# Optimization experiments

Hardware: AMD Instinct MI355X
Metric: run time of the kernel (lower is better)

Reference implementation:

```python
import jax, jax.numpy as jnp
import numpy as np

B, T, D, H, L = 8, 150, 30, 5, 3
HD = D // H  # 6
ORIG = (300, 74, 35)


def setup_inputs() -> dict:
    key = jax.random.key(0)
    ks = iter(jax.random.split(key, 40))
    def g(shape, s=0.05):
        return jax.random.normal(next(ks), shape, dtype=jnp.float32) * s
    return {
        "x_l": g((B, T, ORIG[0]), 1.0),
        "x_a": g((B, T, ORIG[1]), 1.0),
        "x_v": g((B, T, ORIG[2]), 1.0),
        "Wl": g((D, ORIG[0])),
        "Wa": g((D, ORIG[1])),
        "Wv": g((D, ORIG[2])),
        "in_w": g((2, L, 3 * D, D)),
        "in_b": jnp.zeros((2, L, 3 * D), jnp.float32),
        "out_w": g((2, L, D, D)),
        "out_b": jnp.zeros((2, L, D), jnp.float32),
        "lin1_w": g((2, L, 4 * D, D)),
        "lin1_b": jnp.zeros((2, L, 4 * D), jnp.float32),
        "lin2_w": g((2, L, D, 4 * D)),
        "lin2_b": jnp.zeros((2, L, D), jnp.float32),
        "n1_g": jnp.ones((2, L, D), jnp.float32),
        "n1_b": jnp.zeros((2, L, D), jnp.float32),
        "n2_g": jnp.ones((2, L, D), jnp.float32),
        "n2_b": jnp.zeros((2, L, D), jnp.float32),
        "p1_w": g((2 * D, 2 * D)),
        "p1_b": jnp.zeros((2 * D,), jnp.float32),
        "p2_w": g((2 * D, 2 * D)),
        "p2_b": jnp.zeros((2 * D,), jnp.float32),
        "ow": g((1, 2 * D)),
        "ob": jnp.zeros((1,), jnp.float32),
    }


def _ln(x, g, b, eps=1e-5):
    m = x.mean(-1, keepdims=True)
    v = jnp.var(x, axis=-1, keepdims=True)  # biased var, matches torch LayerNorm
    return (x - m) * jax.lax.rsqrt(v + eps) * g + b


def _heads(x):  # [Tt, B, D] -> [B*H, Tt, HD]
    Tt = x.shape[0]
    return x.reshape(Tt, B * H, HD).transpose(1, 0, 2)


def _layer(x, xk, xv, p):
    iw, ib, ow, ob, w1, b1, w2, b2, g1, bb1, g2, bb2 = p
    res = x
    xn, kn, vn = _ln(x, g1, bb1), _ln(xk, g1, bb1), _ln(xv, g1, bb1)
    q = (xn @ iw[:D].T + ib[:D]) * (HD ** -0.5)
    k = kn @ iw[D:2 * D].T + ib[D:2 * D]
    v = vn @ iw[2 * D:].T + ib[2 * D:]
    qh, kh, vh = _heads(q), _heads(k), _heads(v)
    # trilinear scores: [B*H, Tq, Tk, Tv]
    aw = jnp.einsum('iat,ibt,ict->iabc', qh, kh, vh)
    fused = aw.mean(-1) + aw.max(-1)          # fuse over value axis -> [B*H, Tq, Tk]
    fused = jax.nn.softmax(fused, axis=-1)
    attn = jnp.einsum('iab,ibt->iat', fused, qh)  # NB: original bmm uses q, not v
    attn = attn.transpose(1, 0, 2).reshape(-1, B, D)
    x = res + (attn @ ow.T + ob)
    res = x
    xn = _ln(x, g2, bb2)
    x = jax.nn.relu(xn @ w1.T + b1) @ w2.T + b2
    return res + x


def reference(x_l, x_a, x_v, Wl, Wa, Wv, in_w, in_b, out_w, out_b,
              lin1_w, lin1_b, lin2_w, lin2_b, n1_g, n1_b, n2_g, n2_b,
              p1_w, p1_b, p2_w, p2_b, ow, ob):
    pl = (x_l @ Wl.T).transpose(1, 0, 2)  # [T, B, D] (conv1d k=1, no bias)
    pa = (x_a @ Wa.T).transpose(1, 0, 2)
    pv = (x_v @ Wv.T).transpose(1, 0, 2)
    hs = []
    for s, (kk, vv) in enumerate(((pa, pv), (pv, pa))):
        h = pl
        for l in range(L):
            p = (in_w[s, l], in_b[s, l], out_w[s, l], out_b[s, l],
                 lin1_w[s, l], lin1_b[s, l], lin2_w[s, l], lin2_b[s, l],
                 n1_g[s, l], n1_b[s, l], n2_g[s, l], n2_b[s, l])
            h = _layer(h, kk, vv, p)
        hs.append(h[-1])  # last timestep [B, D]
    last_hs = jnp.concatenate(hs, axis=1)  # [B, 2D]
    proj = jax.nn.relu(last_hs @ p1_w.T + p1_b) @ p2_w.T + p2_b + last_hs
    out = proj @ ow.T + ob
    return (out, last_hs)
```

## Files before the change

kernel.cpp:

```cpp
#include <hip/hip_runtime.h>
#include <math.h>

#define BB 8
#define TT 150
#define DD 30
#define HH 5
#define HD 6
#define LL 3
#define NI 40
#define ROWF (TT*BB*DD)
#define RSTR 8
#define NR 152

typedef _Float16 half8 __attribute__((ext_vector_type(8)));
typedef float f32x16 __attribute__((ext_vector_type(16)));

__device__ __forceinline__ float wsum(float v) {
    #pragma unroll
    for (int m = 32; m > 0; m >>= 1) v += __shfl_xor(v, m, 64);
    return v;
}

__global__ __launch_bounds__(256) void proj3_kernel(
    const float* __restrict__ x_l, const float* __restrict__ x_a, const float* __restrict__ x_v,
    const float* __restrict__ Wl, const float* __restrict__ Wa, const float* __restrict__ Wv,
    float* __restrict__ pl, float* __restrict__ pa, float* __restrict__ pv) {
    int w = threadIdx.x >> 6, lane = threadIdx.x & 63;
    int unit = blockIdx.x * 4 + w;
    int which = unit / 1200, rowu = unit % 1200;
    int t = rowu / BB, b = rowu % BB;
    const float* x = which == 0 ? x_l : (which == 1 ? x_a : x_v);
    const float* W = which == 0 ? Wl : (which == 1 ? Wa : Wv);
    float* out = which == 0 ? pl : (which == 1 ? pa : pv);
    int Cin = which == 0 ? 300 : (which == 1 ? 74 : 35);
    __shared__ float xr[4][304];
    const float* xp = x + ((size_t)b * TT + t) * Cin;
    for (int j = lane; j < Cin; j += 64) xr[w][j] = xp[j];
    __syncthreads();
    int d = lane >> 1, jh = lane & 1;
    int h1 = Cin >> 1;
    int j0 = jh ? h1 : 0, j1 = jh ? Cin : h1;
    const float* wr = W + (size_t)(d < DD ? d : 0) * Cin;
    float acc = 0.f;
    for (int j = j0; j < j1; j++) acc += xr[w][j] * wr[j];
    acc += __shfl_xor(acc, 1, 64);
    if (jh == 0 && d < DD) out[t * (BB * DD) + b * DD + d] = acc;
}

__global__ __launch_bounds__(256) void lnqkv_kernel(
    const float* __restrict__ h, const float* __restrict__ pl,
    const float* __restrict__ pa, const float* __restrict__ pv,
    const float* __restrict__ in_w, const float* __restrict__ in_b,
    const float* __restrict__ n1g, const float* __restrict__ n1b, int l,
    float* __restrict__ q, float* __restrict__ k, float* __restrict__ v) {
    int w = threadIdx.x >> 6, lane = threadIdx.x & 63;
    int unit = blockIdx.x * 4 + w;
    int s = unit / 1200, tb = unit % 1200;
    int t = tb / BB, b = tb % BB;
    const float* xk = (s == 0) ? pa : pv;
    const float* xv = (s == 0) ? pv : pa;
    int po = s * LL + l;
    const float* iw = in_w + (size_t)po * 90 * 30;
    const float* ib = in_b + (size_t)po * 90;
    const float* g  = n1g + (size_t)po * 30;
    const float* bbv = n1b + (size_t)po * 30;
    __shared__ float xn[4][3][30];
    const float* rows[3];
    rows[0] = (l == 0) ? (pl + (size_t)tb * 30) : (h + (size_t)s * ROWF + (size_t)tb * 30);
    rows[1] = xk + (size_t)tb * 30;
    rows[2] = xv + (size_t)tb * 30;
    for (int r = 0; r < 3; r++) {
        float xval = (lane < 30) ? rows[r][lane] : 0.f;
        float mean = wsum(xval) * (1.f / 30.f);
        float dv = (lane < 30) ? (xval - mean) : 0.f;
        float var = wsum(dv * dv) * (1.f / 30.f);
        float inv = rsqrtf(var + 1e-5f);
        if (lane < 30) xn[w][r][lane] = dv * inv * g[lane] + bbv[lane];
    }
    __syncthreads();
    for (int o = lane; o < 90; o += 64) {
        int which = o / 30, dd = o % 30;
        const float* wr = iw + o * 30;
        const float* xr = xn[w][which];
        float acc = 0.f;
        #pragma unroll 6
        for (int j = 0; j < 30; j++) acc += wr[j] * xr[j];
        acc += ib[o];
        if (which == 0) acc *= 0.40824829046386307f;
        int i = b * HH + dd / HD, hd = dd % HD;
        float* dst = (which == 0) ? q : ((which == 1) ? k : v);
        dst[((size_t)s * NI + i) * (TT * HD) + t * HD + hd] = acc;
    }
}

__global__ __launch_bounds__(256) void scoreffn_kernel(
    const float* __restrict__ q, const float* __restrict__ k, const float* __restrict__ v,
    const float* __restrict__ pl,
    const float* __restrict__ out_w, const float* __restrict__ out_b,
    const float* __restrict__ l1w, const float* __restrict__ l1b,
    const float* __restrict__ l2w, const float* __restrict__ l2b,
    const float* __restrict__ n2g, const float* __restrict__ n2b, int l,
    float* __restrict__ h) {
    int blk = blockIdx.x;
    int s = blk / 304;
    int rem = blk % 304;
    int b = rem / 38;
    int g = rem % 38;
    int tid = threadIdx.x;
    int wv = tid >> 6, lane = tid & 63;
    int lo = lane & 31, hf = lane >> 5;

    __shared__ __align__(16) _Float16 qsh[HH][NR * RSTR];
    __shared__ __align__(16) _Float16 ksh[HH][NR * RSTR];
    __shared__ __align__(16) _Float16 vsh[HH][NR * RSTR];
    __shared__ float attnS[4][32];
    __shared__ float xnS[4][32];
    __shared__ float hidS[4][128];

    int* qz = (int*)&qsh[0][0];
    int* kz = (int*)&ksh[0][0];
    int* vz = (int*)&vsh[0][0];
    for (int idx = tid; idx < HH * NR * RSTR / 2; idx += 256) {
        qz[idx] = 0; kz[idx] = 0; vz[idx] = 0;
    }
    __syncthreads();
    const float* qg = q + (size_t)(s * NI + b * HH) * (TT * HD);
    const float* kg = k + (size_t)(s * NI + b * HH) * (TT * HD);
    const float* vg = v + (size_t)(s * NI + b * HH) * (TT * HD);
    for (int idx = tid; idx < HH * TT * HD; idx += 256) {
        int h5 = idx / (TT * HD);
        int rr = (idx % (TT * HD)) / HD;
        int t = idx % HD;
        int dst = rr * RSTR + t;
        qsh[h5][dst] = (_Float16)qg[idx];
        ksh[h5][dst] = (_Float16)kg[idx];
        vsh[h5][dst] = (_Float16)vg[idx];
    }
    __syncthreads();
    for (int h5 = wv; h5 < HH; h5 += 4) {
        float v6[6] = {0.f, 0.f, 0.f, 0.f, 0.f, 0.f};
        for (int c = lane; c < TT; c += 64) {
            #pragma unroll
            for (int t = 0; t < 6; t++) v6[t] += (float)vsh[h5][c * RSTR + t];
        }
        #pragma unroll
        for (int m = 32; m > 0; m >>= 1) {
            #pragma unroll
            for (int t = 0; t < 6; t++) v6[t] += __shfl_xor(v6[t], m, 64);
        }
        if (lane < 6) vsh[h5][TT * RSTR + lane] = (_Float16)(v6[lane] * (1.f / TT));
    }
    __syncthreads();

    int a = g * 4 + wv;
    bool alive = (a < TT);

    f32x16 zacc;
    #pragma unroll
    for (int j = 0; j < 16; j++) zacc[j] = 0.f;
    half8 zero8;
    #pragma unroll
    for (int t = 0; t < 8; t++) zero8[t] = (_Float16)0.f;

    if (alive) {
        for (int h5 = 0; h5 < HH; h5++) {
            const _Float16* kbase = qsh[0];
            (void)kbase;
            half8 qav = *(const half8*)&qsh[h5][a * RSTR];
            half8 bfrag[5], afrag[5];
            #pragma unroll
            for (int nt = 0; nt < 5; nt++) {
                int rr = nt * 32 + lo;
                int rc = rr < 151 ? rr : 151;
                half8 kf = *(const half8*)&ksh[h5][rc * RSTR];
                half8 vf = *(const half8*)&vsh[h5][rc * RSTR];
                bfrag[nt] = hf ? zero8 : kf;
                afrag[nt] = hf ? zero8 : (vf * qav);
            }
            float fsc[5];
            #pragma unroll
            for (int nb = 0; nb < 5; nb++) {
                float rm = -INFINITY;
                #pragma unroll
                for (int ma = 0; ma < 4; ma++) {
                    f32x16 acc = __builtin_amdgcn_mfma_f32_32x32x16_f16(afrag[ma], bfrag[nb], zacc, 0, 0, 0);
                    float m = fmaxf(acc[0], acc[1]);
                    #pragma unroll
                    for (int j = 2; j < 16; j += 2) m = fmaxf(fmaxf(m, acc[j]), acc[j + 1]);
                    rm = fmaxf(rm, m);
                }
                f32x16 a4 = __builtin_amdgcn_mfma_f32_32x32x16_f16(afrag[4], bfrag[nb], zacc, 0, 0, 0);
                float m4 = fmaxf(a4[0], a4[1]);
                #pragma unroll
                for (int j = 2; j < 10; j += 2) m4 = fmaxf(fmaxf(m4, a4[j]), a4[j + 1]);
                float ext = (hf == 0) ? fmaxf(a4[10], a4[11]) : -INFINITY;
                rm = fmaxf(rm, fmaxf(m4, ext));
                float om = __shfl_xor(a4[10], 32, 64);
                float mn = hf ? a4[10] : om;
                rm = fmaxf(rm, __shfl_xor(rm, 32, 64));
                int bcol = nb * 32 + lo;
                fsc[nb] = (bcol < TT) ? (mn + rm) : -INFINITY;
            }
            float m = fsc[0];
            #pragma unroll
            for (int nb = 1; nb < 5; nb++) m = fmaxf(m, fsc[nb]);
            #pragma unroll
            for (int msk = 16; msk > 0; msk >>= 1) m = fmaxf(m, __shfl_xor(m, msk, 64));
            float e[5], es = 0.f;
            #pragma unroll
            for (int nb = 0; nb < 5; nb++) { e[nb] = __expf(fsc[nb] - m); es += e[nb]; }
            #pragma unroll
            for (int msk = 16; msk > 0; msk >>= 1) es += __shfl_xor(es, msk, 64);
            float acc6[6] = {0.f, 0.f, 0.f, 0.f, 0.f, 0.f};
            #pragma unroll
            for (int nb = 0; nb < 5; nb++) {
                int bcol = nb * 32 + lo;
                int bi = (bcol < TT) ? bcol : 0;
                float wgt = e[nb];
                half8 qrow = *(const half8*)&qsh[h5][bi * RSTR];
                #pragma unroll
                for (int t = 0; t < 6; t++) acc6[t] += wgt * (float)qrow[t];
            }
            #pragma unroll
            for (int msk = 16; msk > 0; msk >>= 1) {
                #pragma unroll
                for (int t = 0; t < 6; t++) acc6[t] += __shfl_xor(acc6[t], msk, 64);
            }
            if (lane == 0) {
                float inv = 1.f / es;
                #pragma unroll
                for (int t = 0; t < 6; t++) attnS[wv][h5 * 6 + t] = acc6[t] * inv;
            }
        }

        int tb = a * BB + b;
        int po = s * LL + l;
        const float* ow = out_w + (size_t)po * 900;
        const float* ob = out_b + (size_t)po * 30;
        const float* w1 = l1w + (size_t)po * 120 * 30;
        const float* b1 = l1b + (size_t)po * 120;
        const float* w2 = l2w + (size_t)po * 30 * 120;
        const float* b2 = l2b + (size_t)po * 30;
        const float* gg = n2g + (size_t)po * 30;
        const float* bbv = n2b + (size_t)po * 30;
        float* hrow = h + (size_t)s * ROWF + (size_t)tb * 30;
        const float* res = (l == 0) ? (pl + (size_t)tb * 30) : hrow;
        float x1v = 0.f;
        if (lane < 30) {
            const float* wr = ow + lane * 30;
            float acc = 0.f;
            #pragma unroll 6
            for (int j = 0; j < 30; j++) acc += wr[j] * attnS[wv][j];
            x1v = res[lane] + acc + ob[lane];
        }
        float mean = wsum(x1v) * (1.f / 30.f);
        float dv = (lane < 30) ? (x1v - mean) : 0.f;
        float var = wsum(dv * dv) * (1.f / 30.f);
        float inv = rsqrtf(var + 1e-5f);
        if (lane < 30) xnS[wv][lane] = dv * inv * gg[lane] + bbv[lane];
        for (int o = lane; o < 120; o += 64) {
            const float* wr = w1 + o * 30;
            float acc = 0.f;
            #pragma unroll 6
            for (int j = 0; j < 30; j++) acc += wr[j] * xnS[wv][j];
            hidS[wv][o] = fmaxf(acc + b1[o], 0.f);
        }
        if (lane < 30) {
            const float* wr = w2 + lane * 120;
            float acc = 0.f;
            #pragma unroll 8
            for (int j = 0; j < 120; j++) acc += wr[j] * hidS[wv][j];
            hrow[lane] = x1v + acc + b2[lane];
        }
    }
}

__global__ __launch_bounds__(256) void head_kernel(
    const float* __restrict__ h,
    const float* __restrict__ p1w, const float* __restrict__ p1b,
    const float* __restrict__ p2w, const float* __restrict__ p2b,
    const float* __restrict__ ow, const float* __restrict__ ob,
    float* __restrict__ out) {
    int tid = threadIdx.x;
    __shared__ float lh[480], hid[480], pr[480];
    for (int idx = tid; idx < 480; idx += 256) {
        int b = idx / 60, j = idx % 60;
        int s = j / 30, d = j % 30;
        float vv = h[(size_t)s * ROWF + 149 * (BB * DD) + b * DD + d];
        lh[idx] = vv;
        out[8 + idx] = vv;
    }
    __syncthreads();
    for (int idx = tid; idx < 480; idx += 256) {
        int b = idx / 60, o = idx % 60;
        const float* wr = p1w + o * 60;
        float acc = p1b[o];
        for (int j = 0; j < 60; j++) acc += wr[j] * lh[b * 60 + j];
        hid[idx] = fmaxf(acc, 0.f);
    }
    __syncthreads();
    for (int idx = tid; idx < 480; idx += 256) {
        int b = idx / 60, d = idx % 60;
        const float* wr = p2w + d * 60;
        float acc = p2b[d];
        for (int j = 0; j < 60; j++) acc += wr[j] * hid[b * 60 + j];
        pr[idx] = acc + lh[idx];
    }
    __syncthreads();
    if (tid < 8) {
        float acc = ob[0];
        for (int j = 0; j < 60; j++) acc += pr[tid * 60 + j] * ow[j];
        out[tid] = acc;
    }
}

extern "C" void kernel_launch(void* const* d_in, const int* in_sizes, int n_in,
                              void* d_out, int out_size, void* d_ws, size_t ws_size,
                              hipStream_t stream) {
    const float* x_l   = (const float*)d_in[0];
    const float* x_a   = (const float*)d_in[1];
    const float* x_v   = (const float*)d_in[2];
    const float* Wl    = (const float*)d_in[3];
    const float* Wa    = (const float*)d_in[4];
    const float* Wv    = (const float*)d_in[5];
    const float* in_w  = (const float*)d_in[6];
    const float* in_b  = (const float*)d_in[7];
    const float* out_w = (const float*)d_in[8];
    const float* out_b = (const float*)d_in[9];
    const float* l1w   = (const float*)d_in[10];
    const float* l1b   = (const float*)d_in[11];
    const float* l2w   = (const float*)d_in[12];
    const float* l2b   = (const float*)d_in[13];
    const float* n1g   = (const float*)d_in[14];
    const float* n1b   = (const float*)d_in[15];
    const float* n2g   = (const float*)d_in[16];
    const float* n2b   = (const float*)d_in[17];
    const float* p1w   = (const float*)d_in[18];
    const float* p1b   = (const float*)d_in[19];
    const float* p2w   = (const float*)d_in[20];
    const float* p2b   = (const float*)d_in[21];
    const float* oww   = (const float*)d_in[22];
    const float* obb   = (const float*)d_in[23];

    float* ws = (float*)d_ws;
    float* pl = ws;
    float* pa = ws + 36000;
    float* pv = ws + 72000;
    float* h  = ws + 108000;
    float* q  = ws + 180000;
    float* kk = ws + 252000;
    float* vv = ws + 324000;

    proj3_kernel<<<900, 256, 0, stream>>>(x_l, x_a, x_v, Wl, Wa, Wv, pl, pa, pv);

    for (int l = 0; l < LL; l++) {
        lnqkv_kernel<<<600, 256, 0, stream>>>(h, pl, pa, pv, in_w, in_b, n1g, n1b, l, q, kk, vv);
        scoreffn_kernel<<<608, 256, 0, stream>>>(q, kk, vv, pl, out_w, out_b,
                                                 l1w, l1b, l2w, l2b, n2g, n2b, l, h);
    }
    head_kernel<<<1, 256, 0, stream>>>(h, p1w, p1b, p2w, p2b, oww, obb, (float*)d_out);
}
```

Before: 280.4 us.

## Split fused score+FFN kernel into per-head score and FFN kernels; stage weights in LDS

The fused score/FFN kernel is split in two. The score kernel now runs one block per (stream, head, group of 8 query rows), so it loads only one head's Q/K/V into LDS and keeps the K/V fragments in registers across two query rows per wave. A separate FFN kernel reads the attention output from a new workspace buffer. The projection, QKV and FFN kernels also stage their weight matrices in shared memory, padded to avoid bank conflicts. This gives more parallelism and less redundant staging, at the cost of an extra launch per layer and a global round trip for the attention output.

```diff
diff --git a/kernel.cpp b/kernel.cpp
--- a/kernel.cpp
+++ b/kernel.cpp
@@ -25,22 +25,27 @@
     const float* __restrict__ x_l, const float* __restrict__ x_a, const float* __restrict__ x_v,
     const float* __restrict__ Wl, const float* __restrict__ Wa, const float* __restrict__ Wv,
     float* __restrict__ pl, float* __restrict__ pa, float* __restrict__ pv) {
+    int blk = blockIdx.x;
+    int which = blk / 300;
     int w = threadIdx.x >> 6, lane = threadIdx.x & 63;
-    int unit = blockIdx.x * 4 + w;
-    int which = unit / 1200, rowu = unit % 1200;
+    int rowu = (blk % 300) * 4 + w;
     int t = rowu / BB, b = rowu % BB;
     const float* x = which == 0 ? x_l : (which == 1 ? x_a : x_v);
     const float* W = which == 0 ? Wl : (which == 1 ? Wa : Wv);
     float* out = which == 0 ? pl : (which == 1 ? pa : pv);
     int Cin = which == 0 ? 300 : (which == 1 ? 74 : 35);
+    int cst = Cin + ((Cin & 1) ? 0 : 1);
+    __shared__ float WS[30 * 301];
     __shared__ float xr[4][304];
+    for (int j = threadIdx.x; j < DD * Cin; j += 256)
+        WS[(j / Cin) * cst + (j % Cin)] = W[j];
     const float* xp = x + ((size_t)b * TT + t) * Cin;
     for (int j = lane; j < Cin; j += 64) xr[w][j] = xp[j];
     __syncthreads();
     int d = lane >> 1, jh = lane & 1;
     int h1 = Cin >> 1;
     int j0 = jh ? h1 : 0, j1 = jh ? Cin : h1;
-    const float* wr = W + (size_t)(d < DD ? d : 0) * Cin;
+    const float* wr = WS + (size_t)(d < DD ? d : 0) * cst;
     float acc = 0.f;
     for (int j = j0; j < j1; j++) acc += xr[w][j] * wr[j];
     acc += __shfl_xor(acc, 1, 64);
@@ -53,9 +58,10 @@
     const float* __restrict__ in_w, const float* __restrict__ in_b,
     const float* __restrict__ n1g, const float* __restrict__ n1b, int l,
     float* __restrict__ q, float* __restrict__ k, float* __restrict__ v) {
+    int blk = blockIdx.x;
+    int s = blk / 300;
     int w = threadIdx.x >> 6, lane = threadIdx.x & 63;
-    int unit = blockIdx.x * 4 + w;
-    int s = unit / 1200, tb = unit % 1200;
+    int tb = (blk % 300) * 4 + w;
     int t = tb / BB, b = tb % BB;
     const float* xk = (s == 0) ? pa : pv;
     const float* xv = (s == 0) ? pv : pa;
@@ -64,7 +70,9 @@
     const float* ib = in_b + (size_t)po * 90;
     const float* g  = n1g + (size_t)po * 30;
     const float* bbv = n1b + (size_t)po * 30;
+    __shared__ float iwS[2700];
     __shared__ float xn[4][3][30];
+    for (int j = threadIdx.x; j < 2700; j += 256) iwS[j] = iw[j];
     const float* rows[3];
     rows[0] = (l == 0) ? (pl + (size_t)tb * 30) : (h + (size_t)s * ROWF + (size_t)tb * 30);
     rows[1] = xk + (size_t)tb * 30;
@@ -80,7 +88,7 @@
     __syncthreads();
     for (int o = lane; o < 90; o += 64) {
         int which = o / 30, dd = o % 30;
-        const float* wr = iw + o * 30;
+        const float* wr = iwS + o * 30;
         const float* xr = xn[w][which];
         float acc = 0.f;
         #pragma unroll 6
@@ -93,185 +101,195 @@
     }
 }
 
-__global__ __launch_bounds__(256) void scoreffn_kernel(
+__global__ __launch_bounds__(256) void score_kernel(
     const float* __restrict__ q, const float* __restrict__ k, const float* __restrict__ v,
-    const float* __restrict__ pl,
+    float* __restrict__ attn) {
+    int blk = blockIdx.x;
+    int s = blk / 760;
+    int rem = blk % 760;
+    int i = rem / 19;
+    int g = rem % 19;
+    int tid = threadIdx.x;
+    int wv = tid >> 6, lane = tid & 63;
+    int lo = lane & 31, hf = lane >> 5;
+
+    __shared__ __align__(16) _Float16 qsh[NR * RSTR];
+    __shared__ __align__(16) _Float16 ksh[NR * RSTR];
+    __shared__ __align__(16) _Float16 vsh[NR * RSTR];
+
+    int* qz = (int*)qsh; int* kz = (int*)ksh; int* vz = (int*)vsh;
+    for (int idx = tid; idx < NR * RSTR / 2; idx += 256) {
+        qz[idx] = 0; kz[idx] = 0; vz[idx] = 0;
+    }
+    __syncthreads();
+    const float* qg = q + (size_t)(s * NI + i) * (TT * HD);
+    const float* kg = k + (size_t)(s * NI + i) * (TT * HD);
+    const float* vg = v + (size_t)(s * NI + i) * (TT * HD);
+    for (int idx = tid; idx < TT * HD; idx += 256) {
+        int dst = (idx / HD) * RSTR + (idx % HD);
+        qsh[dst] = (_Float16)qg[idx];
+        ksh[dst] = (_Float16)kg[idx];
+        vsh[dst] = (_Float16)vg[idx];
+    }
+    __syncthreads();
+    if (wv == 0) {
+        float v6[6] = {0.f, 0.f, 0.f, 0.f, 0.f, 0.f};
+        for (int c = lane; c < TT; c += 64) {
+            #pragma unroll
+            for (int t = 0; t < 6; t++) v6[t] += (float)vsh[c * RSTR + t];
+        }
+        #pragma unroll
+        for (int m = 32; m > 0; m >>= 1) {
+            #pragma unroll
+            for (int t = 0; t < 6; t++) v6[t] += __shfl_xor(v6[t], m, 64);
+        }
+        if (lane < 6) vsh[TT * RSTR + lane] = (_Float16)(v6[lane] * (1.f / TT));
+    }
+    __syncthreads();
+
+    f32x16 zacc;
+    #pragma unroll
+    for (int j = 0; j < 16; j++) zacc[j] = 0.f;
+    half8 zero8;
+    #pragma unroll
+    for (int t = 0; t < 8; t++) zero8[t] = (_Float16)0.f;
+
+    half8 bfrag[5], vhalf[5];
+    #pragma unroll
+    for (int nt = 0; nt < 5; nt++) {
+        int rr = nt * 32 + lo;
+        int rc = rr < 151 ? rr : 151;
+        half8 kf = *(const half8*)&ksh[rc * RSTR];
+        half8 vf = *(const half8*)&vsh[rc * RSTR];
+        bfrag[nt] = hf ? zero8 : kf;
+        vhalf[nt] = hf ? zero8 : vf;
+    }
+
+    for (int ap = 0; ap < 2; ap++) {
+        int a = g * 8 + wv * 2 + ap;
+        if (a >= TT) break;
+        half8 qav = *(const half8*)&qsh[a * RSTR];
+        half8 afrag[5];
+        #pragma unroll
+        for (int nt = 0; nt < 5; nt++) afrag[nt] = vhalf[nt] * qav;
+
+        float fsc[5];
+        #pragma unroll
+        for (int nb = 0; nb < 5; nb++) {
+            float rm = -INFINITY;
+            #pragma unroll
+            for (int ma = 0; ma < 4; ma++) {
+                f32x16 acc = __builtin_amdgcn_mfma_f32_32x32x16_f16(afrag[ma], bfrag[nb], zacc, 0, 0, 0);
+                float m = fmaxf(acc[0], acc[1]);
+                #pragma unroll
+                for (int j = 2; j < 16; j += 2) m = fmaxf(fmaxf(m, acc[j]), acc[j + 1]);
+                rm = fmaxf(rm, m);
+            }
+            f32x16 a4 = __builtin_amdgcn_mfma_f32_32x32x16_f16(afrag[4], bfrag[nb], zacc, 0, 0, 0);
+            float m4 = fmaxf(a4[0], a4[1]);
+            #pragma unroll
+            for (int j = 2; j < 10; j += 2) m4 = fmaxf(fmaxf(m4, a4[j]), a4[j + 1]);
+            float ext = (hf == 0) ? fmaxf(a4[10], a4[11]) : -INFINITY;
+            rm = fmaxf(rm, fmaxf(m4, ext));
+            float om = __shfl_xor(a4[10], 32, 64);
+            float mn = hf ? a4[10] : om;
+            rm = fmaxf(rm, __shfl_xor(rm, 32, 64));
+            int bcol = nb * 32 + lo;
+            fsc[nb] = (bcol < TT) ? (mn + rm) : -INFINITY;
+        }
+        float m = fsc[0];
+        #pragma unroll
+        for (int nb = 1; nb < 5; nb++) m = fmaxf(m, fsc[nb]);
+        #pragma unroll
+        for (int msk = 16; msk > 0; msk >>= 1) m = fmaxf(m, __shfl_xor(m, msk, 64));
+        float e[5], es = 0.f;
+        #pragma unroll
+        for (int nb = 0; nb < 5; nb++) { e[nb] = __expf(fsc[nb] - m); es += e[nb]; }
+        #pragma unroll
+        for (int msk = 16; msk > 0; msk >>= 1) es += __shfl_xor(es, msk, 64);
+        float acc6[6] = {0.f, 0.f, 0.f, 0.f, 0.f, 0.f};
+        #pragma unroll
+        for (int nb = 0; nb < 5; nb++) {
+            int bcol = nb * 32 + lo;
+            int bi = (bcol < TT) ? bcol : 0;
+            float wgt = e[nb];
+            half8 qrow = *(const half8*)&qsh[bi * RSTR];
+            #pragma unroll
+            for (int t = 0; t < 6; t++) acc6[t] += wgt * (float)qrow[t];
+        }
+        #pragma unroll
+        for (int msk = 16; msk > 0; msk >>= 1) {
+            #pragma unroll
+            for (int t = 0; t < 6; t++) acc6[t] += __shfl_xor(acc6[t], msk, 64);
+        }
+        if (lane == 0) {
+            float inv = 1.f / es;
+            int bo = i / HH, ho = i % HH;
+            float* dst = attn + (size_t)s * ROWF + a * (BB * DD) + bo * DD + ho * HD;
+            #pragma unroll
+            for (int t = 0; t < 6; t++) dst[t] = acc6[t] * inv;
+        }
+    }
+}
+
+__global__ __launch_bounds__(256) void ffn_kernel(
+    const float* __restrict__ attn, const float* __restrict__ pl,
     const float* __restrict__ out_w, const float* __restrict__ out_b,
     const float* __restrict__ l1w, const float* __restrict__ l1b,
     const float* __restrict__ l2w, const float* __restrict__ l2b,
     const float* __restrict__ n2g, const float* __restrict__ n2b, int l,
     float* __restrict__ h) {
     int blk = blockIdx.x;
-    int s = blk / 304;
-    int rem = blk % 304;
-    int b = rem / 38;
-    int g = rem % 38;
-    int tid = threadIdx.x;
-    int wv = tid >> 6, lane = tid & 63;
-    int lo = lane & 31, hf = lane >> 5;
-
-    __shared__ __align__(16) _Float16 qsh[HH][NR * RSTR];
-    __shared__ __align__(16) _Float16 ksh[HH][NR * RSTR];
-    __shared__ __align__(16) _Float16 vsh[HH][NR * RSTR];
-    __shared__ float attnS[4][32];
-    __shared__ float xnS[4][32];
-    __shared__ float hidS[4][128];
-
-    int* qz = (int*)&qsh[0][0];
-    int* kz = (int*)&ksh[0][0];
-    int* vz = (int*)&vsh[0][0];
-    for (int idx = tid; idx < HH * NR * RSTR / 2; idx += 256) {
-        qz[idx] = 0; kz[idx] = 0; vz[idx] = 0;
-    }
-    __syncthreads();
-    const float* qg = q + (size_t)(s * NI + b * HH) * (TT * HD);
-    const float* kg = k + (size_t)(s * NI + b * HH) * (TT * HD);
-    const float* vg = v + (size_t)(s * NI + b * HH) * (TT * HD);
-    for (int idx = tid; idx < HH * TT * HD; idx += 256) {
-        int h5 = idx / (TT * HD);
-        int rr = (idx % (TT * HD)) / HD;
-        int t = idx % HD;
-        int dst = rr * RSTR + t;
-        qsh[h5][dst] = (_Float16)qg[idx];
-        ksh[h5][dst] = (_Float16)kg[idx];
-        vsh[h5][dst] = (_Float16)vg[idx];
-    }
-    __syncthreads();
-    for (int h5 = wv; h5 < HH; h5 += 4) {
-        float v6[6] = {0.f, 0.f, 0.f, 0.f, 0.f, 0.f};
-        for (int c = lane; c < TT; c += 64) {
-            #pragma unroll
-            for (int t = 0; t < 6; t++) v6[t] += (float)vsh[h5][c * RSTR + t];
-        }
-        #pragma unroll
-        for (int m = 32; m > 0; m >>= 1) {
-            #pragma unroll
-            for (int t = 0; t < 6; t++) v6[t] += __shfl_xor(v6[t], m, 64);
-        }
-        if (lane < 6) vsh[h5][TT * RSTR + lane] = (_Float16)(v6[lane] * (1.f / TT));
-    }
-    __syncthreads();
-
-    int a = g * 4 + wv;
-    bool alive = (a < TT);
-
-    f32x16 zacc;
-    #pragma unroll
-    for (int j = 0; j < 16; j++) zacc[j] = 0.f;
-    half8 zero8;
-    #pragma unroll
-    for (int t = 0; t < 8; t++) zero8[t] = (_Float16)0.f;
-
-    if (alive) {
-        for (int h5 = 0; h5 < HH; h5++) {
-            const _Float16* kbase = qsh[0];
-            (void)kbase;
-            half8 qav = *(const half8*)&qsh[h5][a * RSTR];
-            half8 bfrag[5], afrag[5];
-            #pragma unroll
-            for (int nt = 0; nt < 5; nt++) {
-                int rr = nt * 32 + lo;
-                int rc = rr < 151 ? rr : 151;
-                half8 kf = *(const half8*)&ksh[h5][rc * RSTR];
-                half8 vf = *(const half8*)&vsh[h5][rc * RSTR];
-                bfrag[nt] = hf ? zero8 : kf;
-                afrag[nt] = hf ? zero8 : (vf * qav);
-            }
-            float fsc[5];
-            #pragma unroll
-            for (int nb = 0; nb < 5; nb++) {
-                float rm = -INFINITY;
-                #pragma unroll
-                for (int ma = 0; ma < 4; ma++) {
-                    f32x16 acc = __builtin_amdgcn_mfma_f32_32x32x16_f16(afrag[ma], bfrag[nb], zacc, 0, 0, 0);
-                    float m = fmaxf(acc[0], acc[1]);
-                    #pragma unroll
-                    for (int j = 2; j < 16; j += 2) m = fmaxf(fmaxf(m, acc[j]), acc[j + 1]);
-                    rm = fmaxf(rm, m);
-                }
-                f32x16 a4 = __builtin_amdgcn_mfma_f32_32x32x16_f16(afrag[4], bfrag[nb], zacc, 0, 0, 0);
-                float m4 = fmaxf(a4[0], a4[1]);
-                #pragma unroll
-                for (int j = 2; j < 10; j += 2) m4 = fmaxf(fmaxf(m4, a4[j]), a4[j + 1]);
-                float ext = (hf == 0) ? fmaxf(a4[10], a4[11]) : -INFINITY;
-                rm = fmaxf(rm, fmaxf(m4, ext));
-                float om = __shfl_xor(a4[10], 32, 64);
-                float mn = hf ? a4[10] : om;
-                rm = fmaxf(rm, __shfl_xor(rm, 32, 64));
-                int bcol = nb * 32 + lo;
-                fsc[nb] = (bcol < TT) ? (mn + rm) : -INFINITY;
-            }
-            float m = fsc[0];
-            #pragma unroll
-            for (int nb = 1; nb < 5; nb++) m = fmaxf(m, fsc[nb]);
-            #pragma unroll
-            for (int msk = 16; msk > 0; msk >>= 1) m = fmaxf(m, __shfl_xor(m, msk, 64));
-            float e[5], es = 0.f;
-            #pragma unroll
-            for (int nb = 0; nb < 5; nb++) { e[nb] = __expf(fsc[nb] - m); es += e[nb]; }
-            #pragma unroll
-            for (int msk = 16; msk > 0; msk >>= 1) es += __shfl_xor(es, msk, 64);
-            float acc6[6] = {0.f, 0.f, 0.f, 0.f, 0.f, 0.f};
-            #pragma unroll
-            for (int nb = 0; nb < 5; nb++) {
-                int bcol = nb * 32 + lo;
-                int bi = (bcol < TT) ? bcol : 0;
-                float wgt = e[nb];
-                half8 qrow = *(const half8*)&qsh[h5][bi * RSTR];
-                #pragma unroll
-                for (int t = 0; t < 6; t++) acc6[t] += wgt * (float)qrow[t];
-            }
-            #pragma unroll
-            for (int msk = 16; msk > 0; msk >>= 1) {
-                #pragma unroll
-                for (int t = 0; t < 6; t++) acc6[t] += __shfl_xor(acc6[t], msk, 64);
-            }
-            if (lane == 0) {
-                float inv = 1.f / es;
-                #pragma unroll
-                for (int t = 0; t < 6; t++) attnS[wv][h5 * 6 + t] = acc6[t] * inv;
-            }
-        }
-
-        int tb = a * BB + b;
-        int po = s * LL + l;
-        const float* ow = out_w + (size_t)po * 900;
-        const float* ob = out_b + (size_t)po * 30;
-        const float* w1 = l1w + (size_t)po * 120 * 30;
-        const float* b1 = l1b + (size_t)po * 120;
-        const float* w2 = l2w + (size_t)po * 30 * 120;
-        const float* b2 = l2b + (size_t)po * 30;
-        const float* gg = n2g + (size_t)po * 30;
-        const float* bbv = n2b + (size_t)po * 30;
-        float* hrow = h + (size_t)s * ROWF + (size_t)tb * 30;
-        const float* res = (l == 0) ? (pl + (size_t)tb * 30) : hrow;
-        float x1v = 0.f;
-        if (lane < 30) {
-            const float* wr = ow + lane * 30;
-            float acc = 0.f;
-            #pragma unroll 6
-            for (int j = 0; j < 30; j++) acc += wr[j] * attnS[wv][j];
-            x1v = res[lane] + acc + ob[lane];
-        }
-        float mean = wsum(x1v) * (1.f / 30.f);
-        float dv = (lane < 30) ? (x1v - mean) : 0.f;
-        float var = wsum(dv * dv) * (1.f / 30.f);
-        float inv = rsqrtf(var + 1e-5f);
-        if (lane < 30) xnS[wv][lane] = dv * inv * gg[lane] + bbv[lane];
-        for (int o = lane; o < 120; o += 64) {
-            const float* wr = w1 + o * 30;
-            float acc = 0.f;
-            #pragma unroll 6
-            for (int j = 0; j < 30; j++) acc += wr[j] * xnS[wv][j];
-            hidS[wv][o] = fmaxf(acc + b1[o], 0.f);
-        }
-        if (lane < 30) {
-            const float* wr = w2 + lane * 120;
-            float acc = 0.f;
-            #pragma unroll 8
-            for (int j = 0; j < 120; j++) acc += wr[j] * hidS[wv][j];
-            hrow[lane] = x1v + acc + b2[lane];
-        }
+    int s = blk / 300;
+    int w = threadIdx.x >> 6, lane = threadIdx.x & 63;
+    int tb = (blk % 300) * 4 + w;
+    int po = s * LL + l;
+    const float* ow = out_w + (size_t)po * 900;
+    const float* ob = out_b + (size_t)po * 30;
+    const float* w1 = l1w + (size_t)po * 120 * 30;
+    const float* b1 = l1b + (size_t)po * 120;
+    const float* w2 = l2w + (size_t)po * 30 * 120;
+    const float* b2 = l2b + (size_t)po * 30;
+    const float* g  = n2g + (size_t)po * 30;
+    const float* bbv = n2b + (size_t)po * 30;
+    __shared__ float owS[900];
+    __shared__ float w1S[3600];
+    __shared__ float w2S[30 * 121];
+    __shared__ float arS[4][30], xnS[4][32], hidS[4][120];
+    for (int j = threadIdx.x; j < 900; j += 256) owS[j] = ow[j];
+    for (int j = threadIdx.x; j < 3600; j += 256) w1S[j] = w1[j];
+    for (int j = threadIdx.x; j < 3600; j += 256) w2S[(j / 120) * 121 + (j % 120)] = w2[j];
+    __syncthreads();
+    float* hrow = h + (size_t)s * ROWF + (size_t)tb * 30;
+    const float* res = (l == 0) ? (pl + (size_t)tb * 30) : hrow;
+    const float* arow = attn + (size_t)s * ROWF + (size_t)tb * 30;
+    if (lane < 30) arS[w][lane] = arow[lane];
+    float x1v = 0.f;
+    if (lane < 30) {
+        const float* wr = owS + lane * 30;
+        float acc = 0.f;
+        #pragma unroll 6
+        for (int j = 0; j < 30; j++) acc += wr[j] * arS[w][j];
+        x1v = res[lane] + acc + ob[lane];
+    }
+    float mean = wsum(x1v) * (1.f / 30.f);
+    float dv = (lane < 30) ? (x1v - mean) : 0.f;
+    float var = wsum(dv * dv) * (1.f / 30.f);
+    float inv = rsqrtf(var + 1e-5f);
+    if (lane < 30) xnS[w][lane] = dv * inv * g[lane] + bbv[lane];
+    for (int o = lane; o < 120; o += 64) {
+        const float* wr = w1S + o * 30;
+        float acc = 0.f;
+        #pragma unroll 6
+        for (int j = 0; j < 30; j++) acc += wr[j] * xnS[w][j];
+        hidS[w][o] = fmaxf(acc + b1[o], 0.f);
+    }
+    if (lane < 30) {
+        const float* wr = w2S + lane * 121;
+        float acc = 0.f;
+        #pragma unroll 8
+        for (int j = 0; j < 120; j++) acc += wr[j] * hidS[w][j];
+        hrow[lane] = x1v + acc + b2[lane];
     }
 }
 
@@ -350,13 +368,15 @@
     float* q  = ws + 180000;
     float* kk = ws + 252000;
     float* vv = ws + 324000;
+    float* at = ws + 396000;
 
     proj3_kernel<<<900, 256, 0, stream>>>(x_l, x_a, x_v, Wl, Wa, Wv, pl, pa, pv);
 
     for (int l = 0; l < LL; l++) {
         lnqkv_kernel<<<600, 256, 0, stream>>>(h, pl, pa, pv, in_w, in_b, n1g, n1b, l, q, kk, vv);
-        scoreffn_kernel<<<608, 256, 0, stream>>>(q, kk, vv, pl, out_w, out_b,
-                                                 l1w, l1b, l2w, l2b, n2g, n2b, l, h);
+        score_kernel<<<1520, 256, 0, stream>>>(q, kk, vv, at);
+        ffn_kernel<<<600, 256, 0, stream>>>(at, pl, out_w, out_b, l1w, l1b, l2w, l2b,
+                                            n2g, n2b, l, h);
     }
     head_kernel<<<1, 256, 0, stream>>>(h, p1w, p1b, p2w, p2b, oww, obb, (float*)d_out);
 }
```

After: 261.4 us. 1.07x faster.
